# Kernel tuning notes

Hardware: AMD Instinct MI355X
Metric: run time of the kernel (lower is better)

The kernel has to match this reference:

```python
import jax, jax.numpy as jnp
import numpy as np


def setup_inputs() -> dict:
    key = jax.random.key(0)
    ks = jax.random.split(key, 6)
    N, D, B, K, O = 100000, 128, 20000, 32, 128
    features = jax.random.normal(ks[0], (N, D), dtype=jnp.float32)
    raw_features = jax.random.normal(ks[1], (N, D), dtype=jnp.float32)
    W1 = jax.random.normal(ks[2], (D, D), dtype=jnp.float32) * (1.0 / np.sqrt(D))
    b1 = jnp.zeros((D,), dtype=jnp.float32)
    Wn = jax.random.normal(ks[3], (2 * D, O), dtype=jnp.float32) * (1.0 / np.sqrt(2 * D))
    node = jax.random.randint(ks[4], (B, 1), 0, N, dtype=jnp.int64)
    neighbours = jax.random.randint(ks[5], (B, K), 0, N, dtype=jnp.int64)
    return {"features": features, "raw_features": raw_features, "W1": W1,
            "b1": b1, "Wn": Wn, "node": node, "neighbours": neighbours}


def reference(features, raw_features, W1, b1, Wn, node, neighbours):
    # Gather self and neighbor features (irregular access)
    node_feat = features[node[:, 0]]            # [B, D]
    neigh_feat = features[neighbours]           # [B, K, D]
    # Dense + relu applied per neighbor (the single dense layer in build())
    h = jax.nn.relu(jnp.einsum('bkd,de->bke', neigh_feat, W1) + b1)  # [B, K, D]
    # meanpooling over neighbors
    pooled = jnp.mean(h, axis=1)                # [B, D]
    # concat + matmul + relu activation
    out = jax.nn.relu(jnp.concatenate([node_feat, pooled], axis=-1) @ Wn)  # [B, O]
    return (out, raw_features)
```

## Files before the change

### kernel.cpp

```cpp
#include <hip/hip_runtime.h>
#include <hip/hip_bf16.h>
#include <stdint.h>

typedef __bf16 bf16x8 __attribute__((ext_vector_type(8)));
typedef float  f32x4  __attribute__((ext_vector_type(4)));
typedef float  f32x2  __attribute__((ext_vector_type(2)));

#define N_NODES 100000
#define DIM     128
#define B_BATCH 20000
#define K_NB    32
#define O_OUT   128

__global__ void transpose_weights(const float* __restrict__ W1,
                                  const float* __restrict__ Wn,
                                  __bf16* __restrict__ W1t,
                                  __bf16* __restrict__ Wnt) {
    int tid = blockIdx.x * blockDim.x + threadIdx.x;
    if (tid < DIM * DIM) {
        int k = tid >> 7, c = tid & 127;
        W1t[c * DIM + k] = (__bf16)W1[tid];
    }
    int t2 = tid - DIM * DIM;
    if (t2 >= 0 && t2 < 2 * DIM * O_OUT) {
        int k = t2 >> 7, o = t2 & 127;
        Wnt[o * (2 * DIM) + k] = (__bf16)Wn[t2];
    }
}

__global__ __launch_bounds__(256, 4)
void gemm_h(const float* __restrict__ X, const __bf16* __restrict__ W1t,
            const float* __restrict__ b1, __bf16* __restrict__ H) {
    const int lane = threadIdx.x & 63;
    const int wave = threadIdx.x >> 6;
    const int rowbase = blockIdx.x * 64 + wave * 16;
    const int r0 = lane & 15;
    const int kg = lane >> 4;
    int arow = rowbase + r0;
    int arow_c = arow < N_NODES ? arow : 0;

    f32x4 acc[8];
#pragma unroll
    for (int t = 0; t < 8; ++t) acc[t] = (f32x4)0.0f;

#pragma unroll
    for (int k0 = 0; k0 < DIM; k0 += 32) {
        const int k = k0 + kg * 8;
        const float* ap = X + arow_c * DIM + k;
        f32x4 a0 = *(const f32x4*)ap;
        f32x4 a1 = *(const f32x4*)(ap + 4);
        bf16x8 af;
        af[0]=(__bf16)a0[0]; af[1]=(__bf16)a0[1]; af[2]=(__bf16)a0[2]; af[3]=(__bf16)a0[3];
        af[4]=(__bf16)a1[0]; af[5]=(__bf16)a1[1]; af[6]=(__bf16)a1[2]; af[7]=(__bf16)a1[3];
#pragma unroll
        for (int ct = 0; ct < 8; ++ct) {
            const int col = ct * 16 + r0;
            bf16x8 bf = *(const bf16x8*)(W1t + col * DIM + k);
            acc[ct] = __builtin_amdgcn_mfma_f32_16x16x32_bf16(af, bf, acc[ct], 0, 0, 0);
        }
    }
    const int orow_base = rowbase + kg * 4;
#pragma unroll
    for (int ct = 0; ct < 8; ++ct) {
        const int col = ct * 16 + r0;
        const float bias = b1[col];
#pragma unroll
        for (int r = 0; r < 4; ++r) {
            const int row = orow_base + r;
            if (row < N_NODES) {
                float v = acc[ct][r] + bias;
                H[row * DIM + col] = (__bf16)(v > 0.f ? v : 0.f);
            }
        }
    }
}

__global__ __launch_bounds__(256)
void pool_concat(const __bf16* __restrict__ H, const float* __restrict__ X,
                 const int* __restrict__ node, const int* __restrict__ nb,
                 __bf16* __restrict__ Cc) {
    const int lane = threadIdx.x & 63;
    const int wave = threadIdx.x >> 6;
    const int b = blockIdx.x * 4 + wave;

    const int ni = node[b];
    f32x2 nf = *(const f32x2*)(X + (long)ni * DIM + lane * 2);
    union { __bf16 h[2]; uint32_t u; } pk;
    __bf16* crow = Cc + (long)b * 256;
    pk.h[0] = (__bf16)nf[0]; pk.h[1] = (__bf16)nf[1];
    *(uint32_t*)(crow + lane * 2) = pk.u;

    float s0 = 0.f, s1 = 0.f;
    const int* nbp = nb + b * K_NB;
#pragma unroll
    for (int k = 0; k < K_NB; ++k) {
        const int idx = nbp[k];
        uint32_t u = *(const uint32_t*)(H + (long)idx * DIM + lane * 2);
        s0 += __uint_as_float(u << 16);
        s1 += __uint_as_float(u & 0xffff0000u);
    }
    pk.h[0] = (__bf16)(s0 * (1.0f / K_NB));
    pk.h[1] = (__bf16)(s1 * (1.0f / K_NB));
    *(uint32_t*)(crow + 128 + lane * 2) = pk.u;
}

__global__ __launch_bounds__(256, 4)
void gemm_out(const __bf16* __restrict__ Cc, const __bf16* __restrict__ Wnt,
              float* __restrict__ Out) {
    const int lane = threadIdx.x & 63;
    const int wave = threadIdx.x >> 6;
    const int rowbase = blockIdx.x * 64 + wave * 16;
    const int r0 = lane & 15;
    const int kg = lane >> 4;
    int arow = rowbase + r0;
    int arow_c = arow < B_BATCH ? arow : 0;

    f32x4 acc[8];
#pragma unroll
    for (int t = 0; t < 8; ++t) acc[t] = (f32x4)0.0f;

#pragma unroll
    for (int k0 = 0; k0 < 2 * DIM; k0 += 32) {
        const int k = k0 + kg * 8;
        bf16x8 af = *(const bf16x8*)(Cc + (long)arow_c * 256 + k);
#pragma unroll
        for (int ct = 0; ct < 8; ++ct) {
            const int col = ct * 16 + r0;
            bf16x8 bf = *(const bf16x8*)(Wnt + col * 256 + k);
            acc[ct] = __builtin_amdgcn_mfma_f32_16x16x32_bf16(af, bf, acc[ct], 0, 0, 0);
        }
    }
    const int orow_base = rowbase + kg * 4;
#pragma unroll
    for (int ct = 0; ct < 8; ++ct) {
        const int col = ct * 16 + r0;
#pragma unroll
        for (int r = 0; r < 4; ++r) {
            const int row = orow_base + r;
            if (row < B_BATCH) {
                float v = acc[ct][r];
                Out[(long)row * O_OUT + col] = v > 0.f ? v : 0.f;
            }
        }
    }
}

__global__ __launch_bounds__(256)
void copy_raw(const float4* __restrict__ src, float4* __restrict__ dst, int n4) {
    int i = blockIdx.x * blockDim.x + threadIdx.x;
    const int stride = gridDim.x * blockDim.x;
    for (; i < n4; i += stride) dst[i] = src[i];
}

extern "C" void kernel_launch(void* const* d_in, const int* in_sizes, int n_in,
                              void* d_out, int out_size, void* d_ws, size_t ws_size,
                              hipStream_t stream) {
    const float* features = (const float*)d_in[0];
    const float* raw      = (const float*)d_in[1];
    const float* W1       = (const float*)d_in[2];
    const float* b1       = (const float*)d_in[3];
    const float* Wn       = (const float*)d_in[4];
    const int*   node     = (const int*)d_in[5];
    const int*   nb       = (const int*)d_in[6];
    float* out = (float*)d_out;

    char* ws = (char*)d_ws;
    __bf16* H   = (__bf16*)ws;
    __bf16* W1t = (__bf16*)(ws + 25600000);
    __bf16* Wnt = (__bf16*)(ws + 25632768);
    __bf16* Cc  = (__bf16*)(ws + 25698304);

    transpose_weights<<<(DIM*DIM + 2*DIM*O_OUT) / 256, 256, 0, stream>>>(W1, Wn, W1t, Wnt);
    gemm_h<<<(N_NODES + 63) / 64, 256, 0, stream>>>(features, W1t, b1, H);
    pool_concat<<<B_BATCH / 4, 256, 0, stream>>>(H, features, node, nb, Cc);
    gemm_out<<<(B_BATCH + 63) / 64, 256, 0, stream>>>(Cc, Wnt, out);
    copy_raw<<<2048, 256, 0, stream>>>((const float4*)raw,
                                       (float4*)(out + (long)B_BATCH * O_OUT),
                                       N_NODES * DIM / 4);
}
```

Measured before the change: 231.0 us.

## Stage GEMM operands in LDS via async global_load_lds with fragment-ordered weights

Weights are pre-arranged in MFMA fragment order, and both GEMMs stage their X/Cc tile and weights into 64KB of LDS with global_load_lds, using XOR swizzling to avoid bank conflicts. This replaces the strided per-lane global weight loads of the old path. The pooling kernel now loads 16 bytes per lane across 4 neighbour groups and reduces them with shuffles. It also writes Cc in the swizzled layout that gemm_out expects. The cost is lower occupancy (launch bounds 2) and an extra sync/reload phase in gemm_out.

```diff
diff --git a/kernel.cpp b/kernel.cpp
--- a/kernel.cpp
+++ b/kernel.cpp
@@ -12,64 +12,90 @@
 #define K_NB    32
 #define O_OUT   128
 
-__global__ void transpose_weights(const float* __restrict__ W1,
-                                  const float* __restrict__ Wn,
-                                  __bf16* __restrict__ W1t,
-                                  __bf16* __restrict__ Wnt) {
+#define GLOAD16(g, l)  __builtin_amdgcn_global_load_lds(                        \
+    (const __attribute__((address_space(1))) void*)(g),                         \
+    (__attribute__((address_space(3))) void*)(l), 16, 0, 0)
+
+__device__ inline float blo(uint32_t u) { return __uint_as_float(u << 16); }
+__device__ inline float bhi(uint32_t u) { return __uint_as_float(u & 0xffff0000u); }
+
+__global__ void prep_weights(const float* __restrict__ W1,
+                             const float* __restrict__ Wn,
+                             __bf16* __restrict__ W1f,
+                             __bf16* __restrict__ Wnf) {
     int tid = blockIdx.x * blockDim.x + threadIdx.x;
-    if (tid < DIM * DIM) {
-        int k = tid >> 7, c = tid & 127;
-        W1t[c * DIM + k] = (__bf16)W1[tid];
-    }
-    int t2 = tid - DIM * DIM;
-    if (t2 >= 0 && t2 < 2 * DIM * O_OUT) {
-        int k = t2 >> 7, o = t2 & 127;
-        Wnt[o * (2 * DIM) + k] = (__bf16)Wn[t2];
-    }
-}
-
-__global__ __launch_bounds__(256, 4)
-void gemm_h(const float* __restrict__ X, const __bf16* __restrict__ W1t,
+    if (tid < 16384) {
+        int e = tid & 7, l = (tid >> 3) & 63, ct = (tid >> 9) & 7, kt = tid >> 12;
+        int r0 = l & 15, kg = l >> 4;
+        W1f[tid] = (__bf16)W1[(kt * 32 + kg * 8 + e) * DIM + ct * 16 + r0];
+    }
+    int t2 = tid - 16384;
+    if (t2 >= 0 && t2 < 32768) {
+        int e = t2 & 7, l = (t2 >> 3) & 63, ct = (t2 >> 9) & 7, kt = t2 >> 12;
+        int r0 = l & 15, kg = l >> 4;
+        Wnf[t2] = (__bf16)Wn[(kt * 32 + kg * 8 + e) * O_OUT + ct * 16 + r0];
+    }
+}
+
+__global__ __launch_bounds__(256, 2)
+void gemm_h(const float* __restrict__ X, const __bf16* __restrict__ W1f,
             const float* __restrict__ b1, __bf16* __restrict__ H) {
-    const int lane = threadIdx.x & 63;
-    const int wave = threadIdx.x >> 6;
-    const int rowbase = blockIdx.x * 64 + wave * 16;
-    const int r0 = lane & 15;
-    const int kg = lane >> 4;
-    int arow = rowbase + r0;
-    int arow_c = arow < N_NODES ? arow : 0;
+    __shared__ char lds[65536];
+    char* Xs = lds;
+    char* Wf = lds + 32768;
+    const int tid = threadIdx.x;
+    const int lane = tid & 63, wave = tid >> 6;
+    const int r0 = lane & 15, kg = lane >> 4;
+    const long base = (long)blockIdx.x * 64;
+
+#pragma unroll
+    for (int i = 0; i < 8; ++i) {
+        int chunk = i * 256 + wave * 64 + lane;
+        int lrow = chunk >> 5;
+        int coff = (chunk & 31) << 4;
+        long grow = base + lrow; if (grow > N_NODES - 1) grow = N_NODES - 1;
+        const char* g = (const char*)X + grow * 512 + (coff ^ ((lrow & 7) << 4));
+        GLOAD16(g, Xs + chunk * 16);
+    }
+#pragma unroll
+    for (int i = 0; i < 8; ++i) {
+        int chunk = i * 256 + wave * 64 + lane;
+        GLOAD16((const char*)W1f + chunk * 16, Wf + chunk * 16);
+    }
+    __syncthreads();
 
     f32x4 acc[8];
 #pragma unroll
     for (int t = 0; t < 8; ++t) acc[t] = (f32x4)0.0f;
 
-#pragma unroll
-    for (int k0 = 0; k0 < DIM; k0 += 32) {
-        const int k = k0 + kg * 8;
-        const float* ap = X + arow_c * DIM + k;
-        f32x4 a0 = *(const f32x4*)ap;
-        f32x4 a1 = *(const f32x4*)(ap + 4);
+    const int row = wave * 16 + r0;
+    const int swz = (r0 & 7) << 4;
+#pragma unroll
+    for (int kt = 0; kt < 4; ++kt) {
+        const int c0 = kt * 128 + kg * 32;
+        f32x4 a0 = *(const f32x4*)(Xs + row * 512 + (c0 ^ swz));
+        f32x4 a1 = *(const f32x4*)(Xs + row * 512 + ((c0 + 16) ^ swz));
         bf16x8 af;
         af[0]=(__bf16)a0[0]; af[1]=(__bf16)a0[1]; af[2]=(__bf16)a0[2]; af[3]=(__bf16)a0[3];
         af[4]=(__bf16)a1[0]; af[5]=(__bf16)a1[1]; af[6]=(__bf16)a1[2]; af[7]=(__bf16)a1[3];
 #pragma unroll
         for (int ct = 0; ct < 8; ++ct) {
-            const int col = ct * 16 + r0;
-            bf16x8 bf = *(const bf16x8*)(W1t + col * DIM + k);
+            bf16x8 bf = *(const bf16x8*)(Wf + ((kt * 8 + ct) * 64 + lane) * 16);
             acc[ct] = __builtin_amdgcn_mfma_f32_16x16x32_bf16(af, bf, acc[ct], 0, 0, 0);
         }
     }
-    const int orow_base = rowbase + kg * 4;
+
+    const long orow_base = base + wave * 16 + kg * 4;
 #pragma unroll
     for (int ct = 0; ct < 8; ++ct) {
         const int col = ct * 16 + r0;
         const float bias = b1[col];
 #pragma unroll
         for (int r = 0; r < 4; ++r) {
-            const int row = orow_base + r;
-            if (row < N_NODES) {
+            const long orow = orow_base + r;
+            if (orow < N_NODES) {
                 float v = acc[ct][r] + bias;
-                H[row * DIM + col] = (__bf16)(v > 0.f ? v : 0.f);
+                H[orow * DIM + col] = (__bf16)(v > 0.f ? v : 0.f);
             }
         }
     }
@@ -79,67 +105,112 @@
 void pool_concat(const __bf16* __restrict__ H, const float* __restrict__ X,
                  const int* __restrict__ node, const int* __restrict__ nb,
                  __bf16* __restrict__ Cc) {
-    const int lane = threadIdx.x & 63;
-    const int wave = threadIdx.x >> 6;
+    const int lane = threadIdx.x & 63, wave = threadIdx.x >> 6;
     const int b = blockIdx.x * 4 + wave;
+    const int g = lane >> 4, c = lane & 15;
+    const int swz = (b & 7) << 4;
+    char* crow = (char*)Cc + (long)b * 512;
 
     const int ni = node[b];
     f32x2 nf = *(const f32x2*)(X + (long)ni * DIM + lane * 2);
     union { __bf16 h[2]; uint32_t u; } pk;
-    __bf16* crow = Cc + (long)b * 256;
     pk.h[0] = (__bf16)nf[0]; pk.h[1] = (__bf16)nf[1];
-    *(uint32_t*)(crow + lane * 2) = pk.u;
-
-    float s0 = 0.f, s1 = 0.f;
+    *(uint32_t*)(crow + ((lane * 4) ^ swz)) = pk.u;
+
     const int* nbp = nb + b * K_NB;
-#pragma unroll
-    for (int k = 0; k < K_NB; ++k) {
-        const int idx = nbp[k];
-        uint32_t u = *(const uint32_t*)(H + (long)idx * DIM + lane * 2);
-        s0 += __uint_as_float(u << 16);
-        s1 += __uint_as_float(u & 0xffff0000u);
-    }
-    pk.h[0] = (__bf16)(s0 * (1.0f / K_NB));
-    pk.h[1] = (__bf16)(s1 * (1.0f / K_NB));
-    *(uint32_t*)(crow + 128 + lane * 2) = pk.u;
-}
-
-__global__ __launch_bounds__(256, 4)
-void gemm_out(const __bf16* __restrict__ Cc, const __bf16* __restrict__ Wnt,
+    int idx[8];
+#pragma unroll
+    for (int i = 0; i < 8; ++i) idx[i] = nbp[i * 4 + g];
+    float s[8] = {0.f, 0.f, 0.f, 0.f, 0.f, 0.f, 0.f, 0.f};
+#pragma unroll
+    for (int i = 0; i < 8; ++i) {
+        uint4 u = *(const uint4*)(H + (long)idx[i] * DIM + c * 8);
+        s[0] += blo(u.x); s[1] += bhi(u.x);
+        s[2] += blo(u.y); s[3] += bhi(u.y);
+        s[4] += blo(u.z); s[5] += bhi(u.z);
+        s[6] += blo(u.w); s[7] += bhi(u.w);
+    }
+#pragma unroll
+    for (int e = 0; e < 8; ++e) {
+        s[e] += __shfl_xor(s[e], 16);
+        s[e] += __shfl_xor(s[e], 32);
+    }
+    if (g == 0) {
+        union { __bf16 h[8]; uint4 u; } pq;
+#pragma unroll
+        for (int e = 0; e < 8; ++e) pq.h[e] = (__bf16)(s[e] * (1.0f / K_NB));
+        *(uint4*)(crow + ((256 + c * 16) ^ swz)) = pq.u;
+    }
+}
+
+__global__ __launch_bounds__(256, 2)
+void gemm_out(const __bf16* __restrict__ Cc, const __bf16* __restrict__ Wnf,
               float* __restrict__ Out) {
-    const int lane = threadIdx.x & 63;
-    const int wave = threadIdx.x >> 6;
-    const int rowbase = blockIdx.x * 64 + wave * 16;
-    const int r0 = lane & 15;
-    const int kg = lane >> 4;
-    int arow = rowbase + r0;
-    int arow_c = arow < B_BATCH ? arow : 0;
+    __shared__ char lds[65536];
+    char* As = lds;
+    char* Wb = lds + 32768;
+    const int tid = threadIdx.x;
+    const int lane = tid & 63, wave = tid >> 6;
+    const int r0 = lane & 15, kg = lane >> 4;
+    const long base = (long)blockIdx.x * 64;
+
+#pragma unroll
+    for (int i = 0; i < 8; ++i) {
+        int chunk = i * 256 + wave * 64 + lane;
+        int lrow = chunk >> 5;
+        long grow = base + lrow; if (grow > B_BATCH - 1) grow = B_BATCH - 1;
+        const char* g = (const char*)Cc + grow * 512 + ((chunk & 31) << 4);
+        GLOAD16(g, As + chunk * 16);
+    }
+#pragma unroll
+    for (int i = 0; i < 8; ++i) {
+        int chunk = i * 256 + wave * 64 + lane;
+        GLOAD16((const char*)Wnf + chunk * 16, Wb + chunk * 16);
+    }
+    __syncthreads();
 
     f32x4 acc[8];
 #pragma unroll
     for (int t = 0; t < 8; ++t) acc[t] = (f32x4)0.0f;
 
-#pragma unroll
-    for (int k0 = 0; k0 < 2 * DIM; k0 += 32) {
-        const int k = k0 + kg * 8;
-        bf16x8 af = *(const bf16x8*)(Cc + (long)arow_c * 256 + k);
+    const int row = wave * 16 + r0;
+    const int swz = (r0 & 7) << 4;
+#pragma unroll
+    for (int kt = 0; kt < 4; ++kt) {
+        bf16x8 af = *(const bf16x8*)(As + row * 512 + ((kt * 64 + kg * 16) ^ swz));
 #pragma unroll
         for (int ct = 0; ct < 8; ++ct) {
-            const int col = ct * 16 + r0;
-            bf16x8 bf = *(const bf16x8*)(Wnt + col * 256 + k);
+            bf16x8 bf = *(const bf16x8*)(Wb + ((kt * 8 + ct) * 64 + lane) * 16);
             acc[ct] = __builtin_amdgcn_mfma_f32_16x16x32_bf16(af, bf, acc[ct], 0, 0, 0);
         }
     }
-    const int orow_base = rowbase + kg * 4;
+    __syncthreads();
+#pragma unroll
+    for (int i = 0; i < 8; ++i) {
+        int chunk = i * 256 + wave * 64 + lane;
+        GLOAD16((const char*)Wnf + 32768 + chunk * 16, Wb + chunk * 16);
+    }
+    __syncthreads();
+#pragma unroll
+    for (int kt = 4; kt < 8; ++kt) {
+        bf16x8 af = *(const bf16x8*)(As + row * 512 + ((kt * 64 + kg * 16) ^ swz));
+#pragma unroll
+        for (int ct = 0; ct < 8; ++ct) {
+            bf16x8 bf = *(const bf16x8*)(Wb + (((kt - 4) * 8 + ct) * 64 + lane) * 16);
+            acc[ct] = __builtin_amdgcn_mfma_f32_16x16x32_bf16(af, bf, acc[ct], 0, 0, 0);
+        }
+    }
+
+    const long orow_base = base + wave * 16 + kg * 4;
 #pragma unroll
     for (int ct = 0; ct < 8; ++ct) {
         const int col = ct * 16 + r0;
 #pragma unroll
         for (int r = 0; r < 4; ++r) {
-            const int row = orow_base + r;
-            if (row < B_BATCH) {
+            const long orow = orow_base + r;
+            if (orow < B_BATCH) {
                 float v = acc[ct][r];
-                Out[(long)row * O_OUT + col] = v > 0.f ? v : 0.f;
+                Out[orow * O_OUT + col] = v > 0.f ? v : 0.f;
             }
         }
     }
@@ -166,14 +237,14 @@
 
     char* ws = (char*)d_ws;
     __bf16* H   = (__bf16*)ws;
-    __bf16* W1t = (__bf16*)(ws + 25600000);
-    __bf16* Wnt = (__bf16*)(ws + 25632768);
+    __bf16* W1f = (__bf16*)(ws + 25600000);
+    __bf16* Wnf = (__bf16*)(ws + 25632768);
     __bf16* Cc  = (__bf16*)(ws + 25698304);
 
-    transpose_weights<<<(DIM*DIM + 2*DIM*O_OUT) / 256, 256, 0, stream>>>(W1, Wn, W1t, Wnt);
-    gemm_h<<<(N_NODES + 63) / 64, 256, 0, stream>>>(features, W1t, b1, H);
+    prep_weights<<<192, 256, 0, stream>>>(W1, Wn, W1f, Wnf);
+    gemm_h<<<(N_NODES + 63) / 64, 256, 0, stream>>>(features, W1f, b1, H);
     pool_concat<<<B_BATCH / 4, 256, 0, stream>>>(H, features, node, nb, Cc);
-    gemm_out<<<(B_BATCH + 63) / 64, 256, 0, stream>>>(Cc, Wnt, out);
+    gemm_out<<<(B_BATCH + 63) / 64, 256, 0, stream>>>(Cc, Wnf, out);
     copy_raw<<<2048, 256, 0, stream>>>((const float4*)raw,
                                        (float4*)(out + (long)B_BATCH * O_OUT),
                                        N_NODES * DIM / 4);
```

Result: faster. 208.1 us (-9.9%).
